# Performance work log

Hardware: AMD Instinct MI355X
Metric: run time of the kernel (lower is better)

## Reference

```python
import jax, jax.numpy as jnp
import numpy as np

STATE_DIM, ACTION_DIM, HIDDEN_DIM = 12, 4, 16  # hidden_dim must equal state_dim+action_dim
LN_EPS = 1e-5


def setup_inputs() -> dict:
    key = jax.random.key(0)
    ks = jax.random.split(key, 12)
    B, T = 8192, 256
    D = STATE_DIM + ACTION_DIM  # 16
    H = HIDDEN_DIM
    s = 1.0 / np.sqrt(D)
    sh = 1.0 / np.sqrt(H)
    return {
        "initial_state": jax.random.normal(ks[0], (B, 1, STATE_DIM), jnp.float32),
        "commands": jax.random.normal(ks[1], (B, T, ACTION_DIM), jnp.float32),
        "ln_gamma": jnp.ones((D,), jnp.float32),
        "ln_beta": jnp.zeros((D,), jnp.float32),
        "W_in": jax.random.uniform(ks[2], (H, D), jnp.float32, -s, s),
        "b_in": jax.random.uniform(ks[3], (H,), jnp.float32, -s, s),
        "W_ih": jax.random.uniform(ks[4], (4 * H, D), jnp.float32, -sh, sh),  # LSTM input_size = D
        "W_hh": jax.random.uniform(ks[5], (4 * H, H), jnp.float32, -sh, sh),
        "b_ih": jax.random.uniform(ks[6], (4 * H,), jnp.float32, -sh, sh),
        "b_hh": jax.random.uniform(ks[7], (4 * H,), jnp.float32, -sh, sh),
        "W_out": jax.random.uniform(ks[8], (STATE_DIM, H), jnp.float32, -sh, sh),
        "b_out": jax.random.uniform(ks[9], (STATE_DIM,), jnp.float32, -sh, sh),
    }


def _normalize_sincos(state, cos_idx, sin_idx):
    sn, cs = state[:, sin_idx], state[:, cos_idx]
    norm = jnp.sqrt(sn * sn + cs * cs) + 1e-8
    return state.at[:, sin_idx].set(sn / norm).at[:, cos_idx].set(cs / norm)


def _forward(initial_state, commands, ln_gamma, ln_beta, W_in, b_in,
             W_ih, W_hh, b_ih, b_hh, W_out, b_out):
    B = initial_state.shape[0]
    H = W_hh.shape[1]
    state0 = initial_state[:, 0, :]  # (B, S)
    h0 = jnp.zeros((B, H), initial_state.dtype)
    c0 = jnp.zeros((B, H), initial_state.dtype)

    def step(carry, cmd_t):
        state, h, c = carry
        x = jnp.concatenate([state, cmd_t], axis=-1)          # (B, D)
        mu = jnp.mean(x, axis=-1, keepdims=True)
        var = jnp.mean((x - mu) ** 2, axis=-1, keepdims=True)
        x = (x - mu) * jax.lax.rsqrt(var + LN_EPS) * ln_gamma + ln_beta
        x = x @ W_in.T + b_in                                  # (B, H)
        gates = x @ W_ih.T + b_ih + h @ W_hh.T + b_hh          # (B, 4H)
        i, f, g, o = jnp.split(gates, 4, axis=-1)
        c = jax.nn.sigmoid(f) * c + jax.nn.sigmoid(i) * jnp.tanh(g)
        h = jax.nn.sigmoid(o) * jnp.tanh(c)
        state = state + h @ W_out.T + b_out                    # (B, S)
        state = _normalize_sincos(state, 1, 2)
        state = _normalize_sincos(state, 3, 4)
        state = _normalize_sincos(state, 5, 6)
        return (state, h, c), state

    _, outs = jax.lax.scan(step, (state0, h0, c0), jnp.swapaxes(commands, 0, 1))
    return jnp.swapaxes(outs, 0, 1)  # (B, T, S)


def reference(initial_state, commands, ln_gamma, ln_beta, W_in, b_in,
              W_ih, W_hh, b_ih, b_hh, W_out, b_out):
    return _forward(initial_state, commands, ln_gamma, ln_beta, W_in, b_in,
                    W_ih, W_hh, b_ih, b_hh, W_out, b_out)
```

## Files before the change

kernel.cpp:

```cpp
#include <hip/hip_runtime.h>

typedef float f32x2 __attribute__((ext_vector_type(2)));
typedef float f32x4 __attribute__((ext_vector_type(4)));

#define LOG2E 1.44269504088896340736f

__device__ __forceinline__ float rcp_fast(float x) { return __builtin_amdgcn_rcpf(x); }

__device__ __forceinline__ f32x2 mk2(float a, float b) { f32x2 v; v[0] = a; v[1] = b; return v; }

__device__ __forceinline__ float sigmoid_fast(float x) {
    return rcp_fast(1.0f + __builtin_amdgcn_exp2f(-LOG2E * x));
}

__device__ __forceinline__ float tanh_fast(float x) {
    float a = __builtin_fabsf(x);
    float t = __builtin_amdgcn_exp2f(-2.0f * LOG2E * a);
    float r = (1.0f - t) * rcp_fast(1.0f + t);
    return __builtin_copysignf(r, x);
}

__device__ __forceinline__ void load_pairs16(const float* p, f32x2* dst) {
    const f32x4* q4 = (const f32x4*)p;
    f32x4 a = q4[0], b = q4[1], c = q4[2], d = q4[3];
    dst[0] = __builtin_shufflevector(a, a, 0, 1);
    dst[1] = __builtin_shufflevector(a, a, 2, 3);
    dst[2] = __builtin_shufflevector(b, b, 0, 1);
    dst[3] = __builtin_shufflevector(b, b, 2, 3);
    dst[4] = __builtin_shufflevector(c, c, 0, 1);
    dst[5] = __builtin_shufflevector(c, c, 2, 3);
    dst[6] = __builtin_shufflevector(d, d, 0, 1);
    dst[7] = __builtin_shufflevector(d, d, 2, 3);
}

__global__ __launch_bounds__(64) void vm_kernel(
    const float* __restrict__ init_state,
    const float* __restrict__ commands,
    const float* __restrict__ ln_g,
    const float* __restrict__ ln_b,
    const float* __restrict__ W_in,
    const float* __restrict__ b_in,
    const float* __restrict__ W_ih,
    const float* __restrict__ W_hh,
    const float* __restrict__ b_ih,
    const float* __restrict__ b_hh,
    const float* __restrict__ W_out,
    const float* __restrict__ b_out,
    float* __restrict__ out,
    int B, int T)
{
    const int lane = threadIdx.x;
    const int j = lane & 15;
    const int g = lane >> 4;
    const int b = blockIdx.x * 4 + g;

    __shared__ float sh_x[4][20];
    __shared__ float sh_xhh[4][36];
    __shared__ float sh_hn[4][20];

    f32x2 Wg2[8];
    float wbeta;
    float sWg = 0.0f;
    {
        const float* wr = W_in + j * 16;
        float bsum = b_in[j];
        float ssum = 0.0f;
#pragma unroll
        for (int k2 = 0; k2 < 8; ++k2) {
            float w0 = wr[2 * k2], w1 = wr[2 * k2 + 1];
            float g0 = ln_g[2 * k2], g1 = ln_g[2 * k2 + 1];
            float a0 = w0 * g0, a1 = w1 * g1;
            Wg2[k2] = mk2(a0, a1);
            bsum += w0 * ln_b[2 * k2] + w1 * ln_b[2 * k2 + 1];
            ssum += a0 + a1;
        }
        wbeta = bsum;
        sWg = ssum;
    }

    f32x2 Wx[4][8], Wh[4][8];
    float gb[4];
#pragma unroll
    for (int q = 0; q < 4; ++q) {
        const float* rx = W_ih + (q * 16 + j) * 16;
        const float* rh = W_hh + (q * 16 + j) * 16;
#pragma unroll
        for (int k2 = 0; k2 < 8; ++k2) {
            Wx[q][k2] = mk2(rx[2 * k2], rx[2 * k2 + 1]);
            Wh[q][k2] = mk2(rh[2 * k2], rh[2 * k2 + 1]);
        }
        gb[q] = b_ih[q * 16 + j] + b_hh[q * 16 + j];
    }

    f32x2 Wo[8];
    float bo = 0.0f;
#pragma unroll
    for (int k2 = 0; k2 < 8; ++k2) Wo[k2] = mk2(0.0f, 0.0f);
    if (j < 12) {
        const float* ro = W_out + j * 16;
#pragma unroll
        for (int k2 = 0; k2 < 8; ++k2) Wo[k2] = mk2(ro[2 * k2], ro[2 * k2 + 1]);
        bo = b_out[j];
    }

    const bool is_state = (j < 12);
    float st = is_state ? init_state[b * 12 + j] : 0.0f;
    float h = 0.0f, c = 0.0f;

    const float* cmd_ptr = commands + (size_t)b * T * 4 + (j - 12);
    float cmd = (j >= 12) ? cmd_ptr[0] : 0.0f;

    float* out_ptr = out + (size_t)b * T * 12 + j;

    int pj = j;
    if (j >= 1 && j <= 6) pj = ((j - 1) ^ 1) + 1;
    const int psrc = (lane & 48) | pj;
    const bool donorm = (j >= 1 && j <= 6);

    for (int t = 0; t < T; ++t) {
        float x = is_state ? st : cmd;
        sh_x[g][j] = x;

        float cmd_next = 0.0f;
        {
            int tn = (t + 1 < T) ? (t + 1) : t;
            if (j >= 12) cmd_next = cmd_ptr[(size_t)tn * 4];
        }
        __syncthreads();

        f32x2 xp[8];
        load_pairs16(&sh_x[g][0], xp);

        f32x2 s2 = ((xp[0] + xp[1]) + (xp[2] + xp[3])) + ((xp[4] + xp[5]) + (xp[6] + xp[7]));
        float sum = s2[0] + s2[1];
        f32x2 q2 = xp[0] * xp[0];
#pragma unroll
        for (int k2 = 1; k2 < 8; ++k2) q2 += xp[k2] * xp[k2];
        float sumsq = q2[0] + q2[1];
        float mu = sum * 0.0625f;
        float var = sumsq * 0.0625f - mu * mu;
        float inv = __builtin_amdgcn_rsqf(var + 1e-5f);

        f32x2 d2 = Wg2[0] * xp[0];
#pragma unroll
        for (int k2 = 1; k2 < 8; ++k2) d2 += Wg2[k2] * xp[k2];
        float xh = ((d2[0] + d2[1]) - mu * sWg) * inv + wbeta;

        sh_xhh[g][j] = xh;
        sh_xhh[g][16 + j] = h;
        __syncthreads();

        f32x2 ap[8], hp[8];
        load_pairs16(&sh_xhh[g][0], ap);
        load_pairs16(&sh_xhh[g][16], hp);

        f32x2 ai = mk2(0.f, 0.f), af = mk2(0.f, 0.f), ag = mk2(0.f, 0.f), ao = mk2(0.f, 0.f);
#pragma unroll
        for (int k2 = 0; k2 < 8; ++k2) {
            f32x2 xv = ap[k2], hv = hp[k2];
            ai += Wx[0][k2] * xv; af += Wx[1][k2] * xv;
            ag += Wx[2][k2] * xv; ao += Wx[3][k2] * xv;
            ai += Wh[0][k2] * hv; af += Wh[1][k2] * hv;
            ag += Wh[2][k2] * hv; ao += Wh[3][k2] * hv;
        }
        float gi = ai[0] + ai[1] + gb[0];
        float gf = af[0] + af[1] + gb[1];
        float gg = ag[0] + ag[1] + gb[2];
        float go = ao[0] + ao[1] + gb[3];

        float iv = sigmoid_fast(gi);
        float fv = sigmoid_fast(gf);
        float gv = tanh_fast(gg);
        float ov = sigmoid_fast(go);
        c = fv * c + iv * gv;
        h = ov * tanh_fast(c);

        sh_hn[g][j] = h;
        __syncthreads();

        f32x2 hn[8];
        load_pairs16(&sh_hn[g][0], hn);
        f32x2 o2 = Wo[0] * hn[0];
#pragma unroll
        for (int k2 = 1; k2 < 8; ++k2) o2 += Wo[k2] * hn[k2];

        if (is_state) st += (o2[0] + o2[1]) + bo;

        float pv = __shfl(st, psrc, 64);
        if (donorm) {
            float n = __builtin_amdgcn_sqrtf(st * st + pv * pv) + 1e-8f;
            st *= rcp_fast(n);
        }

        if (is_state) out_ptr[0] = st;
        out_ptr += 12;
        cmd = cmd_next;
    }
}

extern "C" void kernel_launch(void* const* d_in, const int* in_sizes, int n_in,
                              void* d_out, int out_size, void* d_ws, size_t ws_size,
                              hipStream_t stream) {
    const float* init_state = (const float*)d_in[0];
    const float* commands   = (const float*)d_in[1];
    const float* ln_g       = (const float*)d_in[2];
    const float* ln_b       = (const float*)d_in[3];
    const float* W_in       = (const float*)d_in[4];
    const float* b_in       = (const float*)d_in[5];
    const float* W_ih       = (const float*)d_in[6];
    const float* W_hh       = (const float*)d_in[7];
    const float* b_ih       = (const float*)d_in[8];
    const float* b_hh       = (const float*)d_in[9];
    const float* W_out      = (const float*)d_in[10];
    const float* b_out      = (const float*)d_in[11];

    int B = in_sizes[0] / 12;
    int T = in_sizes[1] / (B * 4);

    int blocks = B / 4;
    vm_kernel<<<blocks, 64, 0, stream>>>(init_state, commands, ln_g, ln_b,
                                         W_in, b_in, W_ih, W_hh, b_ih, b_hh,
                                         W_out, b_out, (float*)d_out, B, T);
}
```

Baseline: 357.3 us.

## Fold input projection and LayerNorm affine into LSTM gate weights, drop barriers

Precomputes W_ih·W_in with the LayerNorm gamma/beta and all biases folded in. Each step then goes straight from normalized input to gates, which removes a 16x16 matvec and one LDS round-trip. Every lane redoes the sin/cos normalization and LayerNorm statistics from shared memory, and the __syncthreads calls are dropped on the basis that the 64-thread block is a single wavefront. Command loads are prefetched further ahead. The costs are more register pressure from 128 resident gate weights and a reliance on implicit wave-level ordering of LDS accesses.

```diff
diff --git a/kernel.cpp b/kernel.cpp
--- a/kernel.cpp
+++ b/kernel.cpp
@@ -33,7 +33,7 @@
     dst[7] = __builtin_shufflevector(d, d, 2, 3);
 }
 
-__global__ __launch_bounds__(64) void vm_kernel(
+__global__ __launch_bounds__(64, 2) void vm_kernel(
     const float* __restrict__ init_state,
     const float* __restrict__ commands,
     const float* __restrict__ ln_g,
@@ -54,147 +54,175 @@
     const int g = lane >> 4;
     const int b = blockIdx.x * 4 + g;
 
-    __shared__ float sh_x[4][20];
-    __shared__ float sh_xhh[4][36];
-    __shared__ float sh_hn[4][20];
-
-    f32x2 Wg2[8];
-    float wbeta;
-    float sWg = 0.0f;
+    __shared__ __align__(16) float sh_x[4][24];
+    __shared__ __align__(16) float sh_h[4][24];
+
+    f32x2 Wih[4][8], Wh[4][8];
+#pragma unroll
+    for (int q = 0; q < 4; ++q) {
+        load_pairs16(W_ih + (q * 16 + j) * 16, Wih[q]);
+        load_pairs16(W_hh + (q * 16 + j) * 16, Wh[q]);
+    }
+
+    f32x2 Wgx[4][8];
+    float binacc[4];
+#pragma unroll
+    for (int q = 0; q < 4; ++q) {
+        binacc[q] = 0.0f;
+#pragma unroll
+        for (int k2 = 0; k2 < 8; ++k2) Wgx[q][k2] = mk2(0.0f, 0.0f);
+    }
+#pragma unroll
+    for (int m = 0; m < 16; ++m) {
+        f32x2 wm[8];
+        load_pairs16(W_in + m * 16, wm);
+        float bm = b_in[m];
+#pragma unroll
+        for (int q = 0; q < 4; ++q) {
+            float wim = Wih[q][m >> 1][m & 1];
+            f32x2 w2 = mk2(wim, wim);
+#pragma unroll
+            for (int k2 = 0; k2 < 8; ++k2) Wgx[q][k2] += w2 * wm[k2];
+            binacc[q] += wim * bm;
+        }
+    }
+    float sg[4], cst[4];
     {
-        const float* wr = W_in + j * 16;
-        float bsum = b_in[j];
-        float ssum = 0.0f;
-#pragma unroll
-        for (int k2 = 0; k2 < 8; ++k2) {
-            float w0 = wr[2 * k2], w1 = wr[2 * k2 + 1];
-            float g0 = ln_g[2 * k2], g1 = ln_g[2 * k2 + 1];
-            float a0 = w0 * g0, a1 = w1 * g1;
-            Wg2[k2] = mk2(a0, a1);
-            bsum += w0 * ln_b[2 * k2] + w1 * ln_b[2 * k2 + 1];
-            ssum += a0 + a1;
-        }
-        wbeta = bsum;
-        sWg = ssum;
-    }
-
-    f32x2 Wx[4][8], Wh[4][8];
-    float gb[4];
-#pragma unroll
-    for (int q = 0; q < 4; ++q) {
-        const float* rx = W_ih + (q * 16 + j) * 16;
-        const float* rh = W_hh + (q * 16 + j) * 16;
-#pragma unroll
-        for (int k2 = 0; k2 < 8; ++k2) {
-            Wx[q][k2] = mk2(rx[2 * k2], rx[2 * k2 + 1]);
-            Wh[q][k2] = mk2(rh[2 * k2], rh[2 * k2 + 1]);
-        }
-        gb[q] = b_ih[q * 16 + j] + b_hh[q * 16 + j];
-    }
-
+        f32x2 gg2[8], bt2[8];
+        load_pairs16(ln_g, gg2);
+        load_pairs16(ln_b, bt2);
+#pragma unroll
+        for (int q = 0; q < 4; ++q) {
+            f32x2 ss = mk2(0.0f, 0.0f), cc = mk2(0.0f, 0.0f);
+#pragma unroll
+            for (int k2 = 0; k2 < 8; ++k2) {
+                cc += Wgx[q][k2] * bt2[k2];
+                Wgx[q][k2] *= gg2[k2];
+                ss += Wgx[q][k2];
+            }
+            sg[q]  = ss[0] + ss[1];
+            cst[q] = cc[0] + cc[1] + binacc[q] + b_ih[q * 16 + j] + b_hh[q * 16 + j];
+        }
+    }
+
+    const bool is_state = (j < 12);
     f32x2 Wo[8];
     float bo = 0.0f;
 #pragma unroll
     for (int k2 = 0; k2 < 8; ++k2) Wo[k2] = mk2(0.0f, 0.0f);
-    if (j < 12) {
-        const float* ro = W_out + j * 16;
-#pragma unroll
-        for (int k2 = 0; k2 < 8; ++k2) Wo[k2] = mk2(ro[2 * k2], ro[2 * k2 + 1]);
+    if (is_state) {
+        load_pairs16(W_out + j * 16, Wo);
         bo = b_out[j];
     }
 
-    const bool is_state = (j < 12);
     float st = is_state ? init_state[b * 12 + j] : 0.0f;
-    float h = 0.0f, c = 0.0f;
-
-    const float* cmd_ptr = commands + (size_t)b * T * 4 + (j - 12);
-    float cmd = (j >= 12) ? cmd_ptr[0] : 0.0f;
-
+    float c = 0.0f;
+    f32x2 hp[8];
+#pragma unroll
+    for (int k2 = 0; k2 < 8; ++k2) hp[k2] = mk2(0.0f, 0.0f);
+
+    const float* cmd_ptr = commands + (size_t)b * T * 4 + (j >= 12 ? j - 12 : 0);
     float* out_ptr = out + (size_t)b * T * 12 + j;
 
     int pj = j;
     if (j >= 1 && j <= 6) pj = ((j - 1) ^ 1) + 1;
-    const int psrc = (lane & 48) | pj;
+    const float* ppart = &sh_x[g][pj];
     const bool donorm = (j >= 1 && j <= 6);
 
-    for (int t = 0; t < T; ++t) {
-        float x = is_state ? st : cmd;
-        sh_x[g][j] = x;
-
-        float cmd_next = 0.0f;
-        {
-            int tn = (t + 1 < T) ? (t + 1) : t;
-            if (j >= 12) cmd_next = cmd_ptr[(size_t)tn * 4];
-        }
-        __syncthreads();
-
-        f32x2 xp[8];
-        load_pairs16(&sh_x[g][0], xp);
-
+    float cmd0 = (j >= 12) ? cmd_ptr[0] : 0.0f;
+    sh_x[g][j] = is_state ? st : cmd0;
+    f32x2 xp[8];
+    load_pairs16(&sh_x[g][0], xp);
+
+    float mu, inv;
+    {
         f32x2 s2 = ((xp[0] + xp[1]) + (xp[2] + xp[3])) + ((xp[4] + xp[5]) + (xp[6] + xp[7]));
         float sum = s2[0] + s2[1];
-        f32x2 q2 = xp[0] * xp[0];
-#pragma unroll
-        for (int k2 = 1; k2 < 8; ++k2) q2 += xp[k2] * xp[k2];
-        float sumsq = q2[0] + q2[1];
-        float mu = sum * 0.0625f;
+        f32x2 qq = xp[0] * xp[0];
+#pragma unroll
+        for (int k2 = 1; k2 < 8; ++k2) qq += xp[k2] * xp[k2];
+        float sumsq = qq[0] + qq[1];
+        mu = sum * 0.0625f;
         float var = sumsq * 0.0625f - mu * mu;
-        float inv = __builtin_amdgcn_rsqf(var + 1e-5f);
-
-        f32x2 d2 = Wg2[0] * xp[0];
-#pragma unroll
-        for (int k2 = 1; k2 < 8; ++k2) d2 += Wg2[k2] * xp[k2];
-        float xh = ((d2[0] + d2[1]) - mu * sWg) * inv + wbeta;
-
-        sh_xhh[g][j] = xh;
-        sh_xhh[g][16 + j] = h;
-        __syncthreads();
-
-        f32x2 ap[8], hp[8];
-        load_pairs16(&sh_xhh[g][0], ap);
-        load_pairs16(&sh_xhh[g][16], hp);
-
-        f32x2 ai = mk2(0.f, 0.f), af = mk2(0.f, 0.f), ag = mk2(0.f, 0.f), ao = mk2(0.f, 0.f);
-#pragma unroll
-        for (int k2 = 0; k2 < 8; ++k2) {
-            f32x2 xv = ap[k2], hv = hp[k2];
-            ai += Wx[0][k2] * xv; af += Wx[1][k2] * xv;
-            ag += Wx[2][k2] * xv; ao += Wx[3][k2] * xv;
-            ai += Wh[0][k2] * hv; af += Wh[1][k2] * hv;
-            ag += Wh[2][k2] * hv; ao += Wh[3][k2] * hv;
-        }
-        float gi = ai[0] + ai[1] + gb[0];
-        float gf = af[0] + af[1] + gb[1];
-        float gg = ag[0] + ag[1] + gb[2];
-        float go = ao[0] + ao[1] + gb[3];
+        inv = __builtin_amdgcn_rsqf(var + 1e-5f);
+    }
+
+    float cmdS = (j >= 12) ? cmd_ptr[4] : 0.0f;
+    float cmdN = (j >= 12) ? cmd_ptr[8] : 0.0f;
+
+    for (int t = 0; t < T; ++t) {
+        f32x2 ai = Wgx[0][0] * xp[0], af = Wgx[1][0] * xp[0];
+        f32x2 ag = Wgx[2][0] * xp[0], ao = Wgx[3][0] * xp[0];
+        f32x2 hi = Wh[0][0] * hp[0], hf = Wh[1][0] * hp[0];
+        f32x2 hg = Wh[2][0] * hp[0], ho = Wh[3][0] * hp[0];
+#pragma unroll
+        for (int k2 = 1; k2 < 8; ++k2) {
+            ai += Wgx[0][k2] * xp[k2]; af += Wgx[1][k2] * xp[k2];
+            ag += Wgx[2][k2] * xp[k2]; ao += Wgx[3][k2] * xp[k2];
+            hi += Wh[0][k2] * hp[k2];  hf += Wh[1][k2] * hp[k2];
+            hg += Wh[2][k2] * hp[k2];  ho += Wh[3][k2] * hp[k2];
+        }
+        float nmi = -mu * inv;
+        float gi = __builtin_fmaf(ai[0] + ai[1], inv, __builtin_fmaf(nmi, sg[0], cst[0] + (hi[0] + hi[1])));
+        float gf = __builtin_fmaf(af[0] + af[1], inv, __builtin_fmaf(nmi, sg[1], cst[1] + (hf[0] + hf[1])));
+        float gG = __builtin_fmaf(ag[0] + ag[1], inv, __builtin_fmaf(nmi, sg[2], cst[2] + (hg[0] + hg[1])));
+        float go = __builtin_fmaf(ao[0] + ao[1], inv, __builtin_fmaf(nmi, sg[3], cst[3] + (ho[0] + ho[1])));
 
         float iv = sigmoid_fast(gi);
         float fv = sigmoid_fast(gf);
-        float gv = tanh_fast(gg);
+        float gv = tanh_fast(gG);
         float ov = sigmoid_fast(go);
         c = fv * c + iv * gv;
-        h = ov * tanh_fast(c);
-
-        sh_hn[g][j] = h;
-        __syncthreads();
-
-        f32x2 hn[8];
-        load_pairs16(&sh_hn[g][0], hn);
-        f32x2 o2 = Wo[0] * hn[0];
-#pragma unroll
-        for (int k2 = 1; k2 < 8; ++k2) o2 += Wo[k2] * hn[k2];
-
-        if (is_state) st += (o2[0] + o2[1]) + bo;
-
-        float pv = __shfl(st, psrc, 64);
-        if (donorm) {
-            float n = __builtin_amdgcn_sqrtf(st * st + pv * pv) + 1e-8f;
-            st *= rcp_fast(n);
-        }
-
+        float hv = ov * tanh_fast(c);
+
+        sh_h[g][j] = hv;
+        load_pairs16(&sh_h[g][0], hp);
+
+        f32x2 o2 = Wo[0] * hp[0];
+#pragma unroll
+        for (int k2 = 1; k2 < 8; ++k2) o2 += Wo[k2] * hp[k2];
+        float st_raw = st + (o2[0] + o2[1]) + bo;
+
+        sh_x[g][j] = is_state ? st_raw : cmdS;
+        float pv = *ppart;
+        load_pairs16(&sh_x[g][0], xp);
+
+        float nrm = __builtin_amdgcn_sqrtf(st_raw * st_raw + pv * pv) + 1e-8f;
+        float stn = st_raw * rcp_fast(nrm);
+        st = donorm ? stn : st_raw;
         if (is_state) out_ptr[0] = st;
         out_ptr += 12;
-        cmd = cmd_next;
+
+        {
+            float a = xp[0][1], bq = xp[1][0];
+            float r = rcp_fast(__builtin_amdgcn_sqrtf(a * a + bq * bq) + 1e-8f);
+            xp[0][1] = a * r; xp[1][0] = bq * r;
+        }
+        {
+            float a = xp[1][1], bq = xp[2][0];
+            float r = rcp_fast(__builtin_amdgcn_sqrtf(a * a + bq * bq) + 1e-8f);
+            xp[1][1] = a * r; xp[2][0] = bq * r;
+        }
+        {
+            float a = xp[2][1], bq = xp[3][0];
+            float r = rcp_fast(__builtin_amdgcn_sqrtf(a * a + bq * bq) + 1e-8f);
+            xp[2][1] = a * r; xp[3][0] = bq * r;
+        }
+
+        f32x2 s2 = ((xp[0] + xp[1]) + (xp[2] + xp[3])) + ((xp[4] + xp[5]) + (xp[6] + xp[7]));
+        float sum = s2[0] + s2[1];
+        f32x2 qq = xp[0] * xp[0];
+#pragma unroll
+        for (int k2 = 1; k2 < 8; ++k2) qq += xp[k2] * xp[k2];
+        float sumsq = qq[0] + qq[1];
+        mu = sum * 0.0625f;
+        float var = sumsq * 0.0625f - mu * mu;
+        inv = __builtin_amdgcn_rsqf(var + 1e-5f);
+
+        cmdS = cmdN;
+        int tn = t + 3;
+        if (tn > T - 1) tn = T - 1;
+        if (j >= 12) cmdN = cmd_ptr[(size_t)tn * 4];
     }
 }
 
```

Result: no change. 364.1 us (+1.9%).
